# Performance work log

Hardware: AMD Instinct MI355X
Metric: run time of the kernel (lower is better)

The kernel has to match this reference:

```python
import jax, jax.numpy as jnp
import numpy as np

EMBED_DIM = 1024
SEQ_LEN = 2048
BATCH = 8


def setup_inputs() -> dict:
    key = jax.random.key(0)
    ks = jax.random.split(key, 7)
    s = 1.0 / np.sqrt(EMBED_DIM)
    x = jax.random.normal(ks[0], (BATCH, SEQ_LEN, EMBED_DIM), dtype=jnp.float32)
    # torch nn.Linear stores weight as [out, in]; init U(-1/sqrt(in), 1/sqrt(in))
    Wq = jax.random.uniform(ks[1], (EMBED_DIM, EMBED_DIM), jnp.float32, -s, s)
    bq = jax.random.uniform(ks[2], (EMBED_DIM,), jnp.float32, -s, s)
    Wk = jax.random.uniform(ks[3], (EMBED_DIM, EMBED_DIM), jnp.float32, -s, s)
    bk = jax.random.uniform(ks[4], (EMBED_DIM,), jnp.float32, -s, s)
    Wv = jax.random.uniform(ks[5], (EMBED_DIM, EMBED_DIM), jnp.float32, -s, s)
    bv = jax.random.uniform(ks[6], (EMBED_DIM,), jnp.float32, -s, s)
    return {"x": x, "Wq": Wq, "bq": bq, "Wk": Wk, "bk": bk, "Wv": Wv, "bv": bv}


def reference(x, Wq, bq, Wk, bk, Wv, bv):
    # Linear projections (torch Linear: x @ W.T + b)
    q = jnp.einsum("bse,oe->bso", x, Wq) + bq
    k = jnp.einsum("bse,oe->bso", x, Wk) + bk
    v = jnp.einsum("bse,oe->bso", x, Wv) + bv
    scale = 1.0 / jnp.sqrt(jnp.float32(EMBED_DIM))
    sims = jnp.einsum("bqe,bke->bqk", q, k) * scale  # [B, S, S]
    causal = jnp.tril(jnp.ones((SEQ_LEN, SEQ_LEN), dtype=bool))
    masked = jnp.where(causal, sims, jnp.float32(-1e9))
    attn = jax.nn.softmax(masked, axis=2)
    return jnp.einsum("bqk,bke->bqe", attn, v)
```

## Files before the change

kernel.cpp:

```cpp
#include <hip/hip_runtime.h>
#include <hip/hip_bf16.h>
#include <stdint.h>
#include <math.h>

#define DEVI __device__ __forceinline__

typedef __attribute__((ext_vector_type(8))) __bf16    bf16x8;
typedef __attribute__((ext_vector_type(8))) _Float16  f16x8;
typedef __attribute__((ext_vector_type(4))) float     f32x4;

constexpr int BM = 128, BN = 128, BK = 64;

DEVI unsigned int pack2(float a, float b) {
  unsigned short ha = __builtin_bit_cast(unsigned short, __float2bfloat16(a));
  unsigned short hb = __builtin_bit_cast(unsigned short, __float2bfloat16(b));
  return (unsigned int)ha | ((unsigned int)hb << 16);
}

__global__ __launch_bounds__(256) void k_cvt_all(const float* __restrict__ x,
                                                 const float* __restrict__ Wq,
                                                 const float* __restrict__ Wk,
                                                 const float* __restrict__ Wv,
                                                 __hip_bfloat16* __restrict__ xb,
                                                 __hip_bfloat16* __restrict__ Wqb,
                                                 __hip_bfloat16* __restrict__ Wkb,
                                                 __hip_bfloat16* __restrict__ Wvb) {
  int i = blockIdx.x * 256 + threadIdx.x;
  const float* src;
  __hip_bfloat16* dst;
  int k;
  if (i < 4194304) {
    src = x; dst = xb; k = i;
  } else {
    int j = i - 4194304;
    int w = j >> 18;
    k = j & 262143;
    src = (w == 0) ? Wq : (w == 1) ? Wk : Wv;
    dst = (w == 0) ? Wqb : (w == 1) ? Wkb : Wvb;
  }
  float4 f = ((const float4*)src)[k];
  uint2 u;
  u.x = pack2(f.x, f.y);
  u.y = pack2(f.z, f.w);
  ((uint2*)dst)[k] = u;
}

template<int NR>
DEVI void stage_rows(const __hip_bfloat16* gbase, int ld, unsigned short* lds, int tid) {
#pragma unroll
  for (int j = 0; j < NR / 32; ++j) {
    int g   = j * 256 + tid;
    int row = g >> 3;
    int cp  = g & 7;
    int c   = cp ^ (row & 7);
    const __hip_bfloat16* src = gbase + (size_t)row * ld + c * 8;
    unsigned short* dst = lds + (size_t)(j * 256 + (tid & ~63)) * 8;
    __builtin_amdgcn_global_load_lds((__attribute__((address_space(1))) void*)(src),
                                     (__attribute__((address_space(3))) void*)(dst),
                                     16, 0, 0);
  }
}

DEVI void stage_tile(const __hip_bfloat16* gbase, int ld, unsigned short* lds, int tid) {
  stage_rows<128>(gbase, ld, lds, tid);
}

DEVI bf16x8 read_frag(const unsigned short* lds, int row, int kcol) {
  int c  = kcol >> 3;
  int cp = c ^ (row & 7);
  return *(const bf16x8*)(lds + row * 64 + cp * 8);
}

DEVI void gemm_core(unsigned short* sA, unsigned short* sB,
                    const __hip_bfloat16* A0, int lda,
                    const __hip_bfloat16* B0, int ldb,
                    int ktiles, f32x4 (&acc)[4][4]) {
  const int tid  = threadIdx.x;
  const int lane = tid & 63;
  const int wid  = tid >> 6;
  const int quad = lane >> 4;
  const int lr   = lane & 15;
  const int wm   = (wid >> 1) * 64;
  const int wn   = (wid & 1) * 64;
  const f32x4 Z = {0.f, 0.f, 0.f, 0.f};
#pragma unroll
  for (int i = 0; i < 4; ++i)
#pragma unroll
    for (int j = 0; j < 4; ++j) acc[i][j] = Z;

  for (int kt = 0; kt < ktiles; ++kt) {
    stage_tile(A0 + kt * BK, lda, sA, tid);
    stage_tile(B0 + kt * BK, ldb, sB, tid);
    __syncthreads();
#pragma unroll
    for (int ks = 0; ks < BK; ks += 32) {
      bf16x8 af[4], bfr[4];
#pragma unroll
      for (int t = 0; t < 4; ++t) af[t]  = read_frag(sA, wm + t * 16 + lr, ks + quad * 8);
#pragma unroll
      for (int t = 0; t < 4; ++t) bfr[t] = read_frag(sB, wn + t * 16 + lr, ks + quad * 8);
#pragma unroll
      for (int i = 0; i < 4; ++i)
#pragma unroll
        for (int j = 0; j < 4; ++j)
          acc[i][j] = __builtin_amdgcn_mfma_f32_16x16x32_bf16(af[i], bfr[j], acc[i][j], 0, 0, 0);
    }
    __syncthreads();
  }
}

__global__ __launch_bounds__(256, 4) void k_proj_qkv(const __hip_bfloat16* __restrict__ X,
                                                     const __hip_bfloat16* __restrict__ Wq,
                                                     const __hip_bfloat16* __restrict__ Wk,
                                                     const __hip_bfloat16* __restrict__ Wv,
                                                     const float* __restrict__ bq,
                                                     const float* __restrict__ bk,
                                                     const float* __restrict__ bv,
                                                     __hip_bfloat16* __restrict__ Q,
                                                     __hip_bfloat16* __restrict__ Kp,
                                                     __hip_bfloat16* __restrict__ Vt) {
  __shared__ unsigned short sA[BM * BK];
  __shared__ unsigned short sB[BN * BK];
  const int id = blockIdx.x;
  const int w  = id >> 10;
  const int i2 = id & 1023;
  const int mt = ((i2 & 7) << 4) | ((i2 >> 3) & 15);
  const int nt = i2 >> 7;
  const int m0 = mt * BM;
  const int n0 = nt * BN;

  const __hip_bfloat16* W = (w == 0) ? Wq : (w == 1) ? Wk : Wv;
  const float* bias       = (w == 0) ? bq : (w == 1) ? bk : bv;

  f32x4 acc[4][4];
  gemm_core(sA, sB, X + (size_t)m0 * 1024, 1024, W + (size_t)n0 * 1024, 1024, 16, acc);

  const int tid = threadIdx.x, lane = tid & 63, wid = tid >> 6;
  const int quad = lane >> 4, lr = lane & 15;
  const int wm = (wid >> 1) * 64, wn = (wid & 1) * 64;
  float bvv[4];
#pragma unroll
  for (int j = 0; j < 4; ++j) bvv[j] = bias[n0 + wn + j * 16 + lr];

  if (w != 2) {
    __hip_bfloat16* C = (w == 0) ? Q : Kp;
#pragma unroll
    for (int i = 0; i < 4; ++i)
#pragma unroll
      for (int j = 0; j < 4; ++j) {
        int n = n0 + wn + j * 16 + lr;
#pragma unroll
        for (int r = 0; r < 4; ++r) {
          int m = m0 + wm + i * 16 + quad * 4 + r;
          C[(size_t)m * 1024 + n] = __float2bfloat16(acc[i][j][r] + bvv[j]);
        }
      }
  } else {
    const int b = m0 >> 11;
    __hip_bfloat16* Cb = Vt + ((size_t)b << 21);
    const int sb = (m0 & 2047) + wm;
#pragma unroll
    for (int i = 0; i < 4; ++i)
#pragma unroll
      for (int j = 0; j < 4; ++j) {
        int n  = n0 + wn + j * 16 + lr;
        int s0 = sb + i * 16 + quad * 4;
        uint2 u;
        u.x = pack2(acc[i][j][0] + bvv[j], acc[i][j][1] + bvv[j]);
        u.y = pack2(acc[i][j][2] + bvv[j], acc[i][j][3] + bvv[j]);
        *(uint2*)(Cb + (size_t)n * 2048 + s0) = u;
      }
  }
}

__global__ __launch_bounds__(256, 4) void k_scores(const __hip_bfloat16* __restrict__ Q,
                                                   const __hip_bfloat16* __restrict__ Kmat,
                                                   _Float16* __restrict__ S,
                                                   int b0, int zmask, int zshift) {
  __shared__ unsigned short sA[BM * BK];
  __shared__ unsigned short sB[BN * BK];
  const int id = blockIdx.x;
  const int z = id & zmask;
  const int b = b0 + z;
  const int i = id >> zshift;
  int qt = (int)((sqrtf(8.f * (float)i + 1.f) - 1.f) * 0.5f);
  while ((qt + 1) * (qt + 2) / 2 <= i) ++qt;
  while (qt * (qt + 1) / 2 > i) --qt;
  const int kt = i - qt * (qt + 1) / 2;

  const int m0 = qt * BM, n0 = kt * BN;
  f32x4 acc[4][4];
  const __hip_bfloat16* A0 = Q    + ((size_t)b << 21) + (size_t)m0 * 1024;
  const __hip_bfloat16* B0 = Kmat + ((size_t)b << 21) + (size_t)n0 * 1024;
  gemm_core(sA, sB, A0, 1024, B0, 1024, 16, acc);

  _Float16* Sb = S + ((size_t)z << 22);
  const int tid = threadIdx.x, lane = tid & 63, wid = tid >> 6;
  const int quad = lane >> 4, lr = lane & 15;
  const int wm = (wid >> 1) * 64, wn = (wid & 1) * 64;
#pragma unroll
  for (int i2 = 0; i2 < 4; ++i2)
#pragma unroll
    for (int j = 0; j < 4; ++j) {
      int n = n0 + wn + j * 16 + lr;
#pragma unroll
      for (int r = 0; r < 4; ++r) {
        int m = m0 + wm + i2 * 16 + quad * 4 + r;
        Sb[(size_t)m * 2048 + n] = (_Float16)(acc[i2][j][r] * 0.03125f);
      }
    }
}

__global__ __launch_bounds__(256) void k_softmax(_Float16* __restrict__ S) {
  const int wid  = threadIdx.x >> 6;
  const int lane = threadIdx.x & 63;
  const int row  = blockIdx.x * 4 + wid;
  const int q    = row & 2047;
  _Float16* srow = S + ((size_t)row << 11);

  float v[4][8];
  float mx = -1e30f;
#pragma unroll
  for (int it = 0; it < 4; ++it) {
    int k0 = it * 512 + lane * 8;
    if (k0 <= q) {
      f16x8 h = ((const f16x8*)srow)[it * 64 + lane];
#pragma unroll
      for (int i = 0; i < 8; ++i) {
        float f = (float)h[i];
        v[it][i] = (k0 + i <= q) ? f : -1e30f;
        mx = fmaxf(mx, v[it][i]);
      }
    } else {
#pragma unroll
      for (int i = 0; i < 8; ++i) v[it][i] = -1e30f;
    }
  }
#pragma unroll
  for (int off = 32; off > 0; off >>= 1) mx = fmaxf(mx, __shfl_xor(mx, off));

  float e[4][8], s = 0.f;
#pragma unroll
  for (int it = 0; it < 4; ++it)
#pragma unroll
    for (int i = 0; i < 8; ++i) { e[it][i] = __expf(v[it][i] - mx); s += e[it][i]; }
#pragma unroll
  for (int off = 32; off > 0; off >>= 1) s += __shfl_xor(s, off);
  const float inv = 1.0f / s;

#pragma unroll
  for (int it = 0; it < 4; ++it) {
    bf16x8 o;
#pragma unroll
    for (int i = 0; i < 8; ++i) o[i] = (__bf16)(e[it][i] * inv);
    ((bf16x8*)srow)[it * 64 + lane] = o;
  }
}

DEVI void pv_core(unsigned short* sA, unsigned short* sB,
                  const __hip_bfloat16* A0, const __hip_bfloat16* B0,
                  int ktiles, f32x4 (&acc)[4][2]) {
  const int tid  = threadIdx.x;
  const int lane = tid & 63;
  const int wid  = tid >> 6;
  const int quad = lane >> 4;
  const int lr   = lane & 15;
  const int wm   = (wid >> 1) * 64;
  const int wn   = (wid & 1) * 32;
  const f32x4 Z = {0.f, 0.f, 0.f, 0.f};
#pragma unroll
  for (int i = 0; i < 4; ++i)
#pragma unroll
    for (int j = 0; j < 2; ++j) acc[i][j] = Z;

  for (int kt = 0; kt < ktiles; ++kt) {
    stage_rows<128>(A0 + kt * BK, 2048, sA, tid);
    stage_rows<64> (B0 + kt * BK, 2048, sB, tid);
    __syncthreads();
#pragma unroll
    for (int ks = 0; ks < BK; ks += 32) {
      bf16x8 af[4], bfr[2];
#pragma unroll
      for (int t = 0; t < 4; ++t) af[t]  = read_frag(sA, wm + t * 16 + lr, ks + quad * 8);
#pragma unroll
      for (int t = 0; t < 2; ++t) bfr[t] = read_frag(sB, wn + t * 16 + lr, ks + quad * 8);
#pragma unroll
      for (int i = 0; i < 4; ++i)
#pragma unroll
        for (int j = 0; j < 2; ++j)
          acc[i][j] = __builtin_amdgcn_mfma_f32_16x16x32_bf16(af[i], bfr[j], acc[i][j], 0, 0, 0);
    }
    __syncthreads();
  }
}

DEVI void pv_one(unsigned short* sA, unsigned short* sB,
                 const __hip_bfloat16* P, const __hip_bfloat16* VtB,
                 float* Cb, int qt, int nt) {
  const int m0 = qt * BM, n0 = nt * 64;
  const int ktiles = 2 * qt + 2;
  f32x4 acc[4][2];
  pv_core(sA, sB, P + (size_t)m0 * 2048, VtB + (size_t)n0 * 2048, ktiles, acc);

  const int tid = threadIdx.x, lane = tid & 63, wid = tid >> 6;
  const int quad = lane >> 4, lr = lane & 15;
  const int wm = (wid >> 1) * 64, wn = (wid & 1) * 32;
#pragma unroll
  for (int i = 0; i < 4; ++i)
#pragma unroll
    for (int j = 0; j < 2; ++j) {
      int n = n0 + wn + j * 16 + lr;
#pragma unroll
      for (int r = 0; r < 4; ++r) {
        int m = m0 + wm + i * 16 + quad * 4 + r;
        Cb[(size_t)m * 1024 + n] = acc[i][j][r];
      }
    }
}

__global__ __launch_bounds__(256, 4) void k_pv(const _Float16* __restrict__ Sbase,
                                               const __hip_bfloat16* __restrict__ Vt,
                                               float* __restrict__ out,
                                               int b0, int zmask, int zshift) {
  __shared__ unsigned short sA[BM * BK];
  __shared__ unsigned short sB[64 * BK];
  const int id = blockIdx.x;
  const int z = id & zmask;
  const int b = b0 + z;
  const int r2 = id >> zshift;
  const int nt = r2 & 15;
  const int p  = (r2 >> 4) & 7;
  const __hip_bfloat16* P   = (const __hip_bfloat16*)(Sbase + ((size_t)z << 22));
  const __hip_bfloat16* VtB = Vt + ((size_t)b << 21);
  float* Cb = out + ((size_t)b << 21);
  pv_one(sA, sB, P, VtB, Cb, 15 - p, nt);
  pv_one(sA, sB, P, VtB, Cb, p, nt);
}

extern "C" void kernel_launch(void* const* d_in, const int* in_sizes, int n_in,
                              void* d_out, int out_size, void* d_ws, size_t ws_size,
                              hipStream_t stream) {
  const float* x  = (const float*)d_in[0];
  const float* Wq = (const float*)d_in[1];
  const float* bq = (const float*)d_in[2];
  const float* Wk = (const float*)d_in[3];
  const float* bk = (const float*)d_in[4];
  const float* Wv = (const float*)d_in[5];
  const float* bv = (const float*)d_in[6];
  float* out = (float*)d_out;

  char* ws = (char*)d_ws;
  const size_t MB32 = (size_t)33554432;
  const size_t MB64 = (size_t)67108864;

  __hip_bfloat16 *xb, *Wqb, *Wkb, *Wvb, *Q, *Kp, *Vt;
  _Float16* S;
  int G;
  if (ws_size >= (size_t)174063616) {
    S   = (_Float16*)(ws);
    xb  = (__hip_bfloat16*)(ws);
    Wqb = (__hip_bfloat16*)(ws + MB64);
    Wkb = (__hip_bfloat16*)(ws + MB64 + 2097152);
    Wvb = (__hip_bfloat16*)(ws + MB64 + 4194304);
    Q   = (__hip_bfloat16*)(ws + MB64 + 6291456);
    Kp  = (__hip_bfloat16*)(ws + MB64 + 6291456 + MB32);
    Vt  = (__hip_bfloat16*)(ws + MB64 + 6291456 + 2 * MB32);
    G = 8;
  } else {
    S   = (_Float16*)(ws);
    xb  = (__hip_bfloat16*)(ws);
    Wqb = (__hip_bfloat16*)(ws + MB32);
    Wkb = (__hip_bfloat16*)(ws + MB32 + 2097152);
    Wvb = (__hip_bfloat16*)(ws + MB32 + 4194304);
    Q   = (__hip_bfloat16*)(ws + MB32 + 6291456);
    Kp  = (__hip_bfloat16*)(ws + 2 * MB32 + 6291456);
    Vt  = (__hip_bfloat16*)(ws + 3 * MB32 + 6291456);
    G = 4;
  }
  const int zmask  = G - 1;
  const int zshift = (G == 8) ? 3 : 2;

  dim3 blk(256);
  k_cvt_all<<<dim3(19456), blk, 0, stream>>>(x, Wq, Wk, Wv, xb, Wqb, Wkb, Wvb);
  k_proj_qkv<<<dim3(3072), blk, 0, stream>>>(xb, Wqb, Wkb, Wvb, bq, bk, bv, Q, Kp, Vt);

  for (int b0 = 0; b0 < 8; b0 += G) {
    k_scores <<<dim3(G * 136), blk, 0, stream>>>(Q, Kp, S, b0, zmask, zshift);
    k_softmax<<<dim3(G * 512), blk, 0, stream>>>(S);
    k_pv     <<<dim3(G * 128), blk, 0, stream>>>(S, Vt, out, b0, zmask, zshift);
  }
}
```

Baseline: 337.3 us.

## Store causal score matrix as packed lower-triangular 128x128 tiles across all batches

Scores are written into a compact array of only the lower-triangular 128x128 tiles per batch instead of a full 2048x2048 matrix. Softmax and the PV kernel index into this tiled layout, and softmax skips writing masked columns beyond the causal tile range. All eight batches now run in a single launch per stage because the packed buffer fits in a smaller workspace. This cuts wasted memory traffic on the upper triangle, at the cost of more complex address arithmetic and a tighter workspace aliasing plan.

```diff
diff --git a/kernel.cpp b/kernel.cpp
--- a/kernel.cpp
+++ b/kernel.cpp
@@ -10,6 +10,8 @@
 typedef __attribute__((ext_vector_type(4))) float     f32x4;
 
 constexpr int BM = 128, BN = 128, BK = 64;
+constexpr int STILE  = 16384;
+constexpr int SBATCH = 136 * STILE;
 
 DEVI unsigned int pack2(float a, float b) {
   unsigned short ha = __builtin_bit_cast(unsigned short, __float2bfloat16(a));
@@ -175,14 +177,12 @@
 
 __global__ __launch_bounds__(256, 4) void k_scores(const __hip_bfloat16* __restrict__ Q,
                                                    const __hip_bfloat16* __restrict__ Kmat,
-                                                   _Float16* __restrict__ S,
-                                                   int b0, int zmask, int zshift) {
+                                                   _Float16* __restrict__ S) {
   __shared__ unsigned short sA[BM * BK];
   __shared__ unsigned short sB[BN * BK];
   const int id = blockIdx.x;
-  const int z = id & zmask;
-  const int b = b0 + z;
-  const int i = id >> zshift;
+  const int z = id & 7;
+  const int i = id >> 3;
   int qt = (int)((sqrtf(8.f * (float)i + 1.f) - 1.f) * 0.5f);
   while ((qt + 1) * (qt + 2) / 2 <= i) ++qt;
   while (qt * (qt + 1) / 2 > i) --qt;
@@ -190,11 +190,11 @@
 
   const int m0 = qt * BM, n0 = kt * BN;
   f32x4 acc[4][4];
-  const __hip_bfloat16* A0 = Q    + ((size_t)b << 21) + (size_t)m0 * 1024;
-  const __hip_bfloat16* B0 = Kmat + ((size_t)b << 21) + (size_t)n0 * 1024;
+  const __hip_bfloat16* A0 = Q    + ((size_t)z << 21) + (size_t)m0 * 1024;
+  const __hip_bfloat16* B0 = Kmat + ((size_t)z << 21) + (size_t)n0 * 1024;
   gemm_core(sA, sB, A0, 1024, B0, 1024, 16, acc);
 
-  _Float16* Sb = S + ((size_t)z << 22);
+  _Float16* St = S + (size_t)z * SBATCH + (size_t)i * STILE;
   const int tid = threadIdx.x, lane = tid & 63, wid = tid >> 6;
   const int quad = lane >> 4, lr = lane & 15;
   const int wm = (wid >> 1) * 64, wn = (wid & 1) * 64;
@@ -202,33 +202,41 @@
   for (int i2 = 0; i2 < 4; ++i2)
 #pragma unroll
     for (int j = 0; j < 4; ++j) {
-      int n = n0 + wn + j * 16 + lr;
+      int n = wn + j * 16 + lr;
 #pragma unroll
       for (int r = 0; r < 4; ++r) {
-        int m = m0 + wm + i2 * 16 + quad * 4 + r;
-        Sb[(size_t)m * 2048 + n] = (_Float16)(acc[i2][j][r] * 0.03125f);
+        int m = wm + i2 * 16 + quad * 4 + r;
+        St[(size_t)m * 128 + n] = (_Float16)(acc[i2][j][r] * 0.03125f);
       }
     }
 }
 
 __global__ __launch_bounds__(256) void k_softmax(_Float16* __restrict__ S) {
+  const int id   = blockIdx.x;
+  const int z    = id & 7;
+  const int r    = id >> 3;
   const int wid  = threadIdx.x >> 6;
   const int lane = threadIdx.x & 63;
-  const int row  = blockIdx.x * 4 + wid;
-  const int q    = row & 2047;
-  _Float16* srow = S + ((size_t)row << 11);
+  const int q    = r * 4 + wid;
+  const int qt   = q >> 7;
+  const int mr   = q & 127;
+  const int len  = (qt + 1) << 7;
+  const int tri  = (qt * (qt + 1)) >> 1;
+  _Float16* Sz = S + (size_t)z * SBATCH;
 
   float v[4][8];
   float mx = -1e30f;
 #pragma unroll
   for (int it = 0; it < 4; ++it) {
-    int k0 = it * 512 + lane * 8;
-    if (k0 <= q) {
-      f16x8 h = ((const f16x8*)srow)[it * 64 + lane];
+    int c = it * 512 + lane * 8;
+    if (c < len && c <= q) {
+      int kt  = c >> 7;
+      int off = c & 127;
+      f16x8 h = *(const f16x8*)(Sz + (size_t)(tri + kt) * STILE + (size_t)mr * 128 + off);
 #pragma unroll
       for (int i = 0; i < 8; ++i) {
         float f = (float)h[i];
-        v[it][i] = (k0 + i <= q) ? f : -1e30f;
+        v[it][i] = (c + i <= q) ? f : -1e30f;
         mx = fmaxf(mx, v[it][i]);
       }
     } else {
@@ -250,16 +258,22 @@
 
 #pragma unroll
   for (int it = 0; it < 4; ++it) {
-    bf16x8 o;
-#pragma unroll
-    for (int i = 0; i < 8; ++i) o[i] = (__bf16)(e[it][i] * inv);
-    ((bf16x8*)srow)[it * 64 + lane] = o;
+    int c = it * 512 + lane * 8;
+    if (c < len) {
+      bf16x8 o;
+#pragma unroll
+      for (int i = 0; i < 8; ++i) o[i] = (__bf16)(e[it][i] * inv);
+      int kt  = c >> 7;
+      int off = c & 127;
+      *(bf16x8*)(Sz + (size_t)(tri + kt) * STILE + (size_t)mr * 128 + off) = o;
+    }
   }
 }
 
 DEVI void pv_core(unsigned short* sA, unsigned short* sB,
-                  const __hip_bfloat16* A0, const __hip_bfloat16* B0,
-                  int ktiles, f32x4 (&acc)[4][2]) {
+                  const __hip_bfloat16* Pz, int qt,
+                  const __hip_bfloat16* B0,
+                  f32x4 (&acc)[4][2]) {
   const int tid  = threadIdx.x;
   const int lane = tid & 63;
   const int wid  = tid >> 6;
@@ -267,6 +281,8 @@
   const int lr   = lane & 15;
   const int wm   = (wid >> 1) * 64;
   const int wn   = (wid & 1) * 32;
+  const int tri  = (qt * (qt + 1)) >> 1;
+  const int ktiles = 2 * qt + 2;
   const f32x4 Z = {0.f, 0.f, 0.f, 0.f};
 #pragma unroll
   for (int i = 0; i < 4; ++i)
@@ -274,7 +290,8 @@
     for (int j = 0; j < 2; ++j) acc[i][j] = Z;
 
   for (int kt = 0; kt < ktiles; ++kt) {
-    stage_rows<128>(A0 + kt * BK, 2048, sA, tid);
+    const __hip_bfloat16* At = Pz + (size_t)(tri + (kt >> 1)) * STILE + (kt & 1) * 64;
+    stage_rows<128>(At, 128, sA, tid);
     stage_rows<64> (B0 + kt * BK, 2048, sB, tid);
     __syncthreads();
 #pragma unroll
@@ -295,12 +312,11 @@
 }
 
 DEVI void pv_one(unsigned short* sA, unsigned short* sB,
-                 const __hip_bfloat16* P, const __hip_bfloat16* VtB,
+                 const __hip_bfloat16* Pz, const __hip_bfloat16* VtB,
                  float* Cb, int qt, int nt) {
   const int m0 = qt * BM, n0 = nt * 64;
-  const int ktiles = 2 * qt + 2;
   f32x4 acc[4][2];
-  pv_core(sA, sB, P + (size_t)m0 * 2048, VtB + (size_t)n0 * 2048, ktiles, acc);
+  pv_core(sA, sB, Pz, qt, VtB + (size_t)n0 * 2048, acc);
 
   const int tid = threadIdx.x, lane = tid & 63, wid = tid >> 6;
   const int quad = lane >> 4, lr = lane & 15;
@@ -320,21 +336,19 @@
 
 __global__ __launch_bounds__(256, 4) void k_pv(const _Float16* __restrict__ Sbase,
                                                const __hip_bfloat16* __restrict__ Vt,
-                                               float* __restrict__ out,
-                                               int b0, int zmask, int zshift) {
+                                               float* __restrict__ out) {
   __shared__ unsigned short sA[BM * BK];
   __shared__ unsigned short sB[64 * BK];
   const int id = blockIdx.x;
-  const int z = id & zmask;
-  const int b = b0 + z;
-  const int r2 = id >> zshift;
+  const int z = id & 7;
+  const int r2 = id >> 3;
   const int nt = r2 & 15;
   const int p  = (r2 >> 4) & 7;
-  const __hip_bfloat16* P   = (const __hip_bfloat16*)(Sbase + ((size_t)z << 22));
-  const __hip_bfloat16* VtB = Vt + ((size_t)b << 21);
-  float* Cb = out + ((size_t)b << 21);
-  pv_one(sA, sB, P, VtB, Cb, 15 - p, nt);
-  pv_one(sA, sB, P, VtB, Cb, p, nt);
+  const __hip_bfloat16* Pz  = (const __hip_bfloat16*)(Sbase + (size_t)z * SBATCH);
+  const __hip_bfloat16* VtB = Vt + ((size_t)z << 21);
+  float* Cb = out + ((size_t)z << 21);
+  pv_one(sA, sB, Pz, VtB, Cb, 15 - p, nt);
+  pv_one(sA, sB, Pz, VtB, Cb, p, nt);
 }
 
 extern "C" void kernel_launch(void* const* d_in, const int* in_sizes, int n_in,
@@ -351,42 +365,20 @@
 
   char* ws = (char*)d_ws;
   const size_t MB32 = (size_t)33554432;
-  const size_t MB64 = (size_t)67108864;
-
-  __hip_bfloat16 *xb, *Wqb, *Wkb, *Wvb, *Q, *Kp, *Vt;
-  _Float16* S;
-  int G;
-  if (ws_size >= (size_t)174063616) {
-    S   = (_Float16*)(ws);
-    xb  = (__hip_bfloat16*)(ws);
-    Wqb = (__hip_bfloat16*)(ws + MB64);
-    Wkb = (__hip_bfloat16*)(ws + MB64 + 2097152);
-    Wvb = (__hip_bfloat16*)(ws + MB64 + 4194304);
-    Q   = (__hip_bfloat16*)(ws + MB64 + 6291456);
-    Kp  = (__hip_bfloat16*)(ws + MB64 + 6291456 + MB32);
-    Vt  = (__hip_bfloat16*)(ws + MB64 + 6291456 + 2 * MB32);
-    G = 8;
-  } else {
-    S   = (_Float16*)(ws);
-    xb  = (__hip_bfloat16*)(ws);
-    Wqb = (__hip_bfloat16*)(ws + MB32);
-    Wkb = (__hip_bfloat16*)(ws + MB32 + 2097152);
-    Wvb = (__hip_bfloat16*)(ws + MB32 + 4194304);
-    Q   = (__hip_bfloat16*)(ws + MB32 + 6291456);
-    Kp  = (__hip_bfloat16*)(ws + 2 * MB32 + 6291456);
-    Vt  = (__hip_bfloat16*)(ws + 3 * MB32 + 6291456);
-    G = 4;
-  }
-  const int zmask  = G - 1;
-  const int zshift = (G == 8) ? 3 : 2;
+
+  _Float16*       S   = (_Float16*)(ws);
+  __hip_bfloat16* xb  = (__hip_bfloat16*)(ws);
+  __hip_bfloat16* Wqb = (__hip_bfloat16*)(ws + MB32);
+  __hip_bfloat16* Wkb = (__hip_bfloat16*)(ws + MB32 + 2097152);
+  __hip_bfloat16* Wvb = (__hip_bfloat16*)(ws + MB32 + 4194304);
+  __hip_bfloat16* Q   = (__hip_bfloat16*)(ws + MB32 + 6291456);
+  __hip_bfloat16* Kp  = (__hip_bfloat16*)(ws + 2 * MB32 + 6291456);
+  __hip_bfloat16* Vt  = (__hip_bfloat16*)(ws + 3 * MB32 + 6291456);
 
   dim3 blk(256);
   k_cvt_all<<<dim3(19456), blk, 0, stream>>>(x, Wq, Wk, Wv, xb, Wqb, Wkb, Wvb);
   k_proj_qkv<<<dim3(3072), blk, 0, stream>>>(xb, Wqb, Wkb, Wvb, bq, bk, bv, Q, Kp, Vt);
-
-  for (int b0 = 0; b0 < 8; b0 += G) {
-    k_scores <<<dim3(G * 136), blk, 0, stream>>>(Q, Kp, S, b0, zmask, zshift);
-    k_softmax<<<dim3(G * 512), blk, 0, stream>>>(S);
-    k_pv     <<<dim3(G * 128), blk, 0, stream>>>(S, Vt, out, b0, zmask, zshift);
-  }
-}
+  k_scores <<<dim3(8 * 136), blk, 0, stream>>>(Q, Kp, S);
+  k_softmax<<<dim3(8 * 512), blk, 0, stream>>>(S);
+  k_pv     <<<dim3(8 * 128), blk, 0, stream>>>(S, Vt, out);
+}
```

Result: no change. 336.1 us (-0.4%).
